# Performance work log

Measured on AMD Instinct MI355X. Metric: run time of the kernel, lower is better.

The kernel has to match this reference:

```python
import jax, jax.numpy as jnp
import numpy as np
from jax import lax


def _zc_rmsnorm(x, w, eps=1e-6):
    # ZeroCentredRMSNorm: scale is (1 + weight), weight init zeros
    v = jnp.mean(jnp.square(x), -1, keepdims=True)
    return x * lax.rsqrt(v + eps) * (1.0 + w)


def _short_conv(x, w, seg_id):
    # Depthwise causal conv (kernel=4, torch Conv1d tap layout) + silu,
    # respecting packed-segment boundaries (contributions from other
    # segments are masked out, matching varlen causal_conv1d).
    T = x.shape[0]
    out = x * w[:, 3]
    for s in range(1, 4):
        shifted = jnp.pad(x, ((s, 0), (0, 0)))[:T]
        same = jnp.pad(seg_id, (s, 0), constant_values=-1)[:T] == seg_id
        out = out + jnp.where(same[:, None], shifted, 0.0) * w[:, 3 - s]
    return jax.nn.silu(out)


def _l2norm(x, eps=1e-6):
    return x * lax.rsqrt(jnp.sum(jnp.square(x), -1, keepdims=True) + eps)


def _forward(x, ac_table, W_in, b_in, norm_w, Wq, Wk, Wv, conv_qw, conv_kw,
             conv_vw, Wb, Wa, A_log, dt_bias, Wg, o_norm_w, Wo, W_head, b_head,
             cu_seqlens, aircraft_type_idx):
    T = x.shape[0]
    NH = A_log.shape[0]
    # segment id per packed token
    seg_id = jnp.searchsorted(cu_seqlens, jnp.arange(T), side='right') - 1
    ac = ac_table[aircraft_type_idx]                    # [S, AC_D]
    h = jnp.concatenate([x, ac[seg_id]], axis=1) @ W_in + b_in  # [T, H]
    residual = h
    hn = _zc_rmsnorm(h, norm_w)
    # GatedDeltaNet projections + short conv + silu
    q = _short_conv(hn @ Wq, conv_qw, seg_id)           # [T, KD]
    k = _short_conv(hn @ Wk, conv_kw, seg_id)           # [T, KD]
    v = _short_conv(hn @ Wv, conv_vw, seg_id)           # [T, VD]
    HK = q.shape[1] // NH
    HV = v.shape[1] // NH
    q = _l2norm(q.reshape(T, NH, HK))
    k = _l2norm(k.reshape(T, NH, HK))
    v = v.reshape(T, NH, HV)
    beta = jax.nn.sigmoid(hn @ Wb)                      # [T, NH]
    g = -jnp.exp(A_log) * jax.nn.softplus(hn @ Wa + dt_bias)  # [T, NH] log-decay
    scale = HK ** -0.5
    # reset flag: 1.0 at the first token of each segment
    starts = jnp.zeros((T,), jnp.float32).at[cu_seqlens[:-1]].set(1.0)

    def step(S, inp):
        qt, kt, vt, gt, bt, rt = inp
        S = S * (1.0 - rt) * jnp.exp(gt)[:, None, None]       # decay (+ reset)
        kv = jnp.einsum('hk,hkv->hv', kt, S)                   # S^T k
        S = S + kt[:, :, None] * (bt[:, None] * (vt - kv))[:, None, :]
        return S, jnp.einsum('hk,hkv->hv', qt, S)

    S0 = jnp.zeros((NH, HK, HV), jnp.float32)
    _, o = lax.scan(step, S0, (q * scale, k, v, g, beta, starts))  # o: [T,NH,HV]
    # swish-gated RMSNorm on output heads
    gate = (hn @ Wg).reshape(T, NH, HV)
    o = o * lax.rsqrt(jnp.mean(jnp.square(o), -1, keepdims=True) + 1e-5) * o_norm_w
    o = o * gate * jax.nn.sigmoid(gate)
    h = o.reshape(T, NH * HV) @ Wo + residual
    pooled = h[cu_seqlens[1:] - 1]                      # 'last' pooling
    return pooled @ W_head + b_head                     # [S, 1]


def setup_inputs() -> dict:
    T, D_IN, H, NH, AC_N, AC_D, S = 32768, 16, 1024, 12, 64, 32, 16
    KD = int(H * 0.75)          # 768
    VD = KD * 2                 # 1536 (expand_v = 2)
    HK, HV = KD // NH, VD // NH # 64, 128
    rng = np.random.default_rng(0)
    interior = np.sort(rng.choice(np.arange(1, T), S - 1, replace=False))
    cu = jnp.asarray(np.concatenate([[0], interior, [T]]).astype(np.int32))
    ks = jax.random.split(jax.random.key(0), 24)

    def n(i, shape, s=0.02):
        return jax.random.normal(ks[i], shape, jnp.float32) * s

    return dict(
        x=jax.random.normal(ks[0], (T, D_IN), jnp.float32),
        cu_seqlens=cu,
        aircraft_type_idx=jax.random.randint(ks[1], (S,), 0, AC_N),
        ac_table=n(2, (AC_N, AC_D), 1.0),
        W_in=n(3, (D_IN + AC_D, H)), b_in=jnp.zeros((H,), jnp.float32),
        norm_w=jnp.zeros((H,), jnp.float32),
        Wq=n(4, (H, KD)), Wk=n(5, (H, KD)), Wv=n(6, (H, VD)),
        conv_qw=n(7, (KD, 4), 0.2), conv_kw=n(8, (KD, 4), 0.2),
        conv_vw=n(9, (VD, 4), 0.2),
        Wb=n(10, (H, NH)), Wa=n(11, (H, NH)),
        A_log=jnp.log(jax.random.uniform(ks[12], (NH,), jnp.float32, 1.0, 16.0)),
        dt_bias=n(13, (NH,), 0.1),
        Wg=n(14, (H, VD)), o_norm_w=jnp.ones((HV,), jnp.float32),
        Wo=n(15, (VD, H)),
        W_head=n(16, (H, 1)), b_head=jnp.zeros((1,), jnp.float32),
    )


def reference(x, cu_seqlens, aircraft_type_idx, ac_table, W_in, b_in, norm_w,
              Wq, Wk, Wv, conv_qw, conv_kw, conv_vw, Wb, Wa, A_log, dt_bias,
              Wg, o_norm_w, Wo, W_head, b_head):
    return _forward(x, ac_table, W_in, b_in, norm_w, Wq, Wk, Wv, conv_qw,
                    conv_kw, conv_vw, Wb, Wa, A_log, dt_bias, Wg, o_norm_w,
                    Wo, W_head, b_head, cu_seqlens, aircraft_type_idx)
```

## Files before the change

kernel.cpp:

```cpp
#include <hip/hip_runtime.h>
#include <stdint.h>

#define T_TOK 32768
#define H_DIM 1024
#define NH    12
#define HK    64
#define HV    128
#define KD    768
#define VD    1536
#define NSEG  16
#define NCOL  2432
#define FEAT  48
#define CHUNK_M 4096
#define NSLOT (T_TOK/8 + 32)
#define MAXSB 96
#define OCH   8

typedef unsigned int uint;
typedef unsigned short ushort;

typedef short bf16x8_t __attribute__((ext_vector_type(8)));
typedef float f32x4_t  __attribute__((ext_vector_type(4)));

__device__ __forceinline__ ushort f2b(float f){
  uint u = __float_as_uint(f);
  u += 0x7fffu + ((u>>16)&1u);
  return (ushort)(u>>16);
}
__device__ __forceinline__ float b2f(ushort u){ return __uint_as_float(((uint)u)<<16); }
__device__ __forceinline__ void unpack2(uint u, float&a, float&b){
  a = __uint_as_float(u<<16); b = __uint_as_float(u & 0xffff0000u);
}
__device__ __forceinline__ float sigm(float x){ return 1.f/(1.f + __expf(-x)); }
__device__ __forceinline__ float silu(float x){ return x * sigm(x); }

__global__ void segk(const int* __restrict__ cu, int* __restrict__ seg){
  int t = blockIdx.x*256 + threadIdx.x;
  if (t >= T_TOK) return;
  int s = 0;
  #pragma unroll
  for (int i=1;i<=NSEG;i++) s += (cu[i] <= t) ? 1 : 0;
  seg[t] = s;
}

__global__ __launch_bounds__(256,1) void stage_a(const float* __restrict__ x,
   const int* __restrict__ atype, const float* __restrict__ ac_table,
   const float* __restrict__ W_in, const float* __restrict__ b_in,
   const float* __restrict__ norm_w, const int* __restrict__ seg, int row_base,
   ushort* __restrict__ hn, float* __restrict__ h_end, float* __restrict__ hn_ends)
{
  __shared__ float feat[8][FEAT];
  __shared__ float hbuf[8][H_DIM];
  __shared__ float red[8];
  int tid = threadIdx.x;
  int base = row_base + blockIdx.x*8;
  int lbase = blockIdx.x*8;
  if (tid < 8) red[tid] = 0.f;
  for (int idx=tid; idx<8*FEAT; idx+=256){
    int rr = idx / FEAT, i = idx % FEAT;
    int t = base + rr;
    float v;
    if (i < 16) v = x[t*16 + i];
    else { int s = seg[t]; int a = atype[s]; v = ac_table[a*32 + (i-16)]; }
    feat[rr][i] = v;
  }
  __syncthreads();
  int c0 = tid*4;
  int lane = tid & 63;
  float4 bi = *(const float4*)&b_in[c0];
  for (int rc=0; rc<2; rc++){
    float acc[4][4];
    #pragma unroll
    for (int r4=0;r4<4;r4++){ acc[r4][0]=bi.x; acc[r4][1]=bi.y; acc[r4][2]=bi.z; acc[r4][3]=bi.w; }
    for (int i=0;i<FEAT;i++){
      float4 wu = *(const float4*)&W_in[i*H_DIM + c0];
      #pragma unroll
      for (int r4=0;r4<4;r4++){
        float f = feat[rc*4+r4][i];
        acc[r4][0] = fmaf(f,wu.x,acc[r4][0]);
        acc[r4][1] = fmaf(f,wu.y,acc[r4][1]);
        acc[r4][2] = fmaf(f,wu.z,acc[r4][2]);
        acc[r4][3] = fmaf(f,wu.w,acc[r4][3]);
      }
    }
    #pragma unroll
    for (int r4=0;r4<4;r4++){
      int rr = rc*4+r4;
      float sq = acc[r4][0]*acc[r4][0] + acc[r4][1]*acc[r4][1]
               + acc[r4][2]*acc[r4][2] + acc[r4][3]*acc[r4][3];
      #pragma unroll
      for (int off=1; off<64; off<<=1) sq += __shfl_xor(sq, off);
      if (lane==0) atomicAdd(&red[rr], sq);
      hbuf[rr][c0]=acc[r4][0]; hbuf[rr][c0+1]=acc[r4][1];
      hbuf[rr][c0+2]=acc[r4][2]; hbuf[rr][c0+3]=acc[r4][3];
    }
  }
  __syncthreads();
  float4 nw = *(const float4*)&norm_w[c0];
  for (int rr=0; rr<8; rr++){
    int t = base + rr;
    float sc = rsqrtf(red[rr]*(1.f/1024.f) + 1e-6f);
    float h0=hbuf[rr][c0], h1=hbuf[rr][c0+1], h2=hbuf[rr][c0+2], h3=hbuf[rr][c0+3];
    float n0=h0*sc*(1.f+nw.x), n1=h1*sc*(1.f+nw.y);
    float n2=h2*sc*(1.f+nw.z), n3=h3*sc*(1.f+nw.w);
    uint2 ov; ov.x = (uint)f2b(n0) | ((uint)f2b(n1)<<16);
    ov.y = (uint)f2b(n2) | ((uint)f2b(n3)<<16);
    *(uint2*)&hn[(size_t)(lbase+rr)*H_DIM + c0] = ov;
    int sgt = seg[t];
    bool isend = (t == T_TOK-1) || (seg[t+1] != sgt);
    if (isend){
      float* he = h_end + (size_t)sgt*H_DIM + c0;
      he[0]=h0; he[1]=h1; he[2]=h2; he[3]=h3;
    }
    #pragma unroll
    for (int d=0; d<4; d++){
      int td = t + d;
      if (td < T_TOK && seg[td] == sgt){
        bool end2 = (td == T_TOK-1) || (seg[td+1] != sgt);
        if (end2){
          float* hd = hn_ends + ((size_t)sgt*4 + (3-d))*H_DIM + c0;
          hd[0]=n0; hd[1]=n1; hd[2]=n2; hd[3]=n3;
        }
      }
    }
  }
}

__global__ void build_wt(const float* __restrict__ Wk, const float* __restrict__ Wv,
                         const float* __restrict__ Wb, const float* __restrict__ Wa,
                         ushort* __restrict__ wt)
{
  int idx = blockIdx.x*256 + threadIdx.x;
  int n = idx >> 10, k = idx & 1023;
  float v;
  if      (n < 768)  v = Wk[k*768 + n];
  else if (n < 2304) v = Wv[k*1536 + (n-768)];
  else if (n < 2316) v = Wb[k*12 + (n-2304)];
  else if (n < 2328) v = Wa[k*12 + (n-2316)];
  else               v = 0.f;
  wt[idx] = f2b(v);
}

__global__ __launch_bounds__(256,1) void gemm_bf16(const ushort* __restrict__ A,
    const ushort* __restrict__ Bt, int row_base,
    ushort* __restrict__ kpre, ushort* __restrict__ vpre, float* __restrict__ ba)
{
  const int K = H_DIM;
  __shared__ ushort As[128*40];
  __shared__ ushort Bs[128*40];
  int tid = threadIdx.x;
  const int ntile = NCOL >> 7;
  int mt = blockIdx.x / ntile, nt = blockIdx.x % ntile;
  int m0 = mt<<7, n0 = nt<<7;
  int r = tid>>2, c8 = (tid&3)<<3;
  const ushort* pa0 = A  + (size_t)(m0 + r)*K + c8;
  const ushort* pa1 = A  + (size_t)(m0 + r + 64)*K + c8;
  const ushort* pb0 = Bt + (size_t)(n0 + r)*K + c8;
  const ushort* pb1 = Bt + (size_t)(n0 + r + 64)*K + c8;
  int lane = tid & 63;
  int wv = tid >> 6; int wm = (wv>>1)<<6, wn = (wv&1)<<6;
  int mloc = lane & 15, q8 = (lane>>4)<<3;
  f32x4_t acc[4][4];
  f32x4_t zero = {0.f,0.f,0.f,0.f};
  #pragma unroll
  for (int i=0;i<4;i++)
    #pragma unroll
    for (int j=0;j<4;j++) acc[i][j] = zero;
  for (int kk=0; kk<K; kk+=32){
    uint4 a0 = *(const uint4*)(pa0 + kk);
    uint4 a1 = *(const uint4*)(pa1 + kk);
    uint4 b0 = *(const uint4*)(pb0 + kk);
    uint4 b1 = *(const uint4*)(pb1 + kk);
    __syncthreads();
    *(uint4*)&As[r*40 + c8] = a0;
    *(uint4*)&As[(r+64)*40 + c8] = a1;
    *(uint4*)&Bs[r*40 + c8] = b0;
    *(uint4*)&Bs[(r+64)*40 + c8] = b1;
    __syncthreads();
    bf16x8_t af[4], bfr[4];
    #pragma unroll
    for (int i=0;i<4;i++){
      af[i]  = *(const bf16x8_t*)&As[(wm + i*16 + mloc)*40 + q8];
      bfr[i] = *(const bf16x8_t*)&Bs[(wn + i*16 + mloc)*40 + q8];
    }
    #pragma unroll
    for (int i=0;i<4;i++)
      #pragma unroll
      for (int j=0;j<4;j++)
        acc[i][j] = __builtin_amdgcn_mfma_f32_16x16x32_bf16(af[i], bfr[j], acc[i][j], 0,0,0);
  }
  int rq = (lane>>4)<<2;
  if (nt < 18){
    ushort* dst; int nstr, cbase;
    if (nt < 6) { dst = kpre; nstr = KD; cbase = n0; }
    else        { dst = vpre; nstr = VD; cbase = n0 - KD; }
    #pragma unroll
    for (int i=0;i<4;i++){
      #pragma unroll
      for (int j=0;j<4;j++){
        int colg = cbase + wn + j*16 + mloc;
        #pragma unroll
        for (int rg=0; rg<4; rg++){
          int rowg = row_base + m0 + wm + i*16 + rq + rg;
          dst[(size_t)rowg*nstr + colg] = f2b(acc[i][j][rg]);
        }
      }
    }
  } else {
    #pragma unroll
    for (int i=0;i<4;i++){
      #pragma unroll
      for (int j=0;j<4;j++){
        int cl = wn + j*16 + mloc;
        if (cl >= 24) continue;
        #pragma unroll
        for (int rg=0; rg<4; rg++){
          int rowg = row_base + m0 + wm + i*16 + rq + rg;
          ba[(size_t)rowg*32 + cl] = acc[i][j][rg];
        }
      }
    }
  }
}

__global__ void dbk(const float* __restrict__ ba, const float* __restrict__ A_log,
                    const float* __restrict__ dt_bias, float2* __restrict__ db)
{
  int idx = blockIdx.x*256 + threadIdx.x;
  if (idx >= T_TOK*NH) return;
  int t = idx / NH, hh = idx % NH;
  float bp = ba[(size_t)t*32 + hh];
  float ap = ba[(size_t)t*32 + 12 + hh] + dt_bias[hh];
  float beta = sigm(bp);
  float sp = (ap > 20.f) ? ap : log1pf(__expf(ap));
  float dec = __expf(-__expf(A_log[hh]) * sp);
  float2 o; o.x = dec; o.y = beta;
  db[idx] = o;
}

__global__ void side_k(const ushort* __restrict__ kpre, const ushort* __restrict__ vpre,
                       ushort* __restrict__ side)
{
  int b = blockIdx.x;
  int base = b*64;
  for (int idx=threadIdx.x; idx<3*2304; idx+=256){
    int jrow = idx / 2304, c = idx % 2304;
    int t0 = base - 3 + jrow;
    ushort v = 0;
    if (t0 >= 0)
      v = (c < KD) ? kpre[(size_t)t0*KD + c] : vpre[(size_t)t0*VD + (c-KD)];
    side[(size_t)(b*3 + jrow)*2304 + c] = v;
  }
}

__global__ __launch_bounds__(256,1) void conv_ip(ushort* __restrict__ kpre,
   ushort* __restrict__ vpre, const ushort* __restrict__ side,
   const int* __restrict__ seg, const float* __restrict__ ckw, const float* __restrict__ cvw)
{
  int tid = threadIdx.x;
  int b = blockIdx.x;
  int base = b * 64;
  float w[9][4];
  int cj[9];
  #pragma unroll
  for (int j=0;j<9;j++){
    int c = tid + 256*j;
    cj[j] = c;
    float4 wu = (c < KD) ? *(const float4*)&ckw[c*4] : *(const float4*)&cvw[(c-KD)*4];
    w[j][0]=wu.x; w[j][1]=wu.y; w[j][2]=wu.z; w[j][3]=wu.w;
  }
  float p[9][4];
  #pragma unroll
  for (int j=0;j<9;j++){
    p[j][1] = b2f(side[(size_t)(b*3+0)*2304 + cj[j]]);
    p[j][2] = b2f(side[(size_t)(b*3+1)*2304 + cj[j]]);
    p[j][3] = b2f(side[(size_t)(b*3+2)*2304 + cj[j]]);
  }
  int s1 = (base-3>=0) ? seg[base-3] : -1;
  int s2 = (base-2>=0) ? seg[base-2] : -1;
  int s3 = (base-1>=0) ? seg[base-1] : -1;
  int s0;
  for (int rr=0; rr<64; rr++){
    int t = base + rr;
    s0 = s1; s1 = s2; s2 = s3; s3 = seg[t];
    #pragma unroll
    for (int j=0;j<9;j++){
      p[j][0]=p[j][1]; p[j][1]=p[j][2]; p[j][2]=p[j][3];
      int c = cj[j];
      p[j][3] = (c < KD) ? b2f(kpre[(size_t)t*KD + c]) : b2f(vpre[(size_t)t*VD + (c-KD)]);
    }
    bool m0 = (s0==s3), m1 = (s1==s3), m2 = (s2==s3);
    #pragma unroll
    for (int j=0;j<9;j++){
      float val = p[j][3]*w[j][3];
      val += m2 ? p[j][2]*w[j][2] : 0.f;
      val += m1 ? p[j][1]*w[j][1] : 0.f;
      val += m0 ? p[j][0]*w[j][0] : 0.f;
      val = silu(val);
      int c = cj[j];
      if (j < 3){
        float sq = val*val;
        #pragma unroll
        for (int off=1; off<64; off<<=1) sq += __shfl_xor(sq, off);
        float kn = val * rsqrtf(sq + 1e-6f);
        kpre[(size_t)t*KD + c] = f2b(kn);
      } else {
        vpre[(size_t)t*VD + (c-KD)] = f2b(val);
      }
    }
  }
}

__global__ __launch_bounds__(256,1) void qpre_k(const float* __restrict__ hn_ends,
   const float* __restrict__ Wq, const int* __restrict__ cu, float* __restrict__ qpre)
{
  __shared__ float hrow[H_DIM];
  int tid = threadIdx.x;
  int s = blockIdx.x >> 2, rr = blockIdx.x & 3;
  int t = cu[s+1] - 4 + rr;
  if (t >= 0)
    *(float4*)&hrow[tid*4] = *(const float4*)&hn_ends[(size_t)(s*4+rr)*H_DIM + tid*4];
  __syncthreads();
  for (int j=0;j<3;j++){
    int c = tid + 256*j;
    float acc = 0.f;
    if (t >= 0){
      for (int i0=0; i0<H_DIM; i0++)
        acc = fmaf(hrow[i0], Wq[(size_t)i0*KD + c], acc);
    }
    qpre[(size_t)(s*4+rr)*KD + c] = acc;
  }
}

__global__ __launch_bounds__(256,1) void qfin_k(const float* __restrict__ qpre,
   const float* __restrict__ cqw, const int* __restrict__ cu, const int* __restrict__ seg,
   float* __restrict__ qf)
{
  int tid = threadIdx.x;
  int s = blockIdx.x;
  int te = cu[s+1]-1;
  for (int j=0;j<3;j++){
    int c = tid + 256*j;
    float4 wu = *(const float4*)&cqw[c*4];
    float wv_[4] = {wu.x, wu.y, wu.z, wu.w};
    float val = 0.f;
    #pragma unroll
    for (int rr=0; rr<4; rr++){
      int t = te - 3 + rr;
      bool ok = (t >= 0) && (seg[t] == s);
      float pv = qpre[(size_t)(s*4+rr)*KD + c];
      val += ok ? pv * wv_[rr] : 0.f;
    }
    val = silu(val);
    float sq = val*val;
    #pragma unroll
    for (int off=1; off<64; off<<=1) sq += __shfl_xor(sq, off);
    qf[(size_t)s*KD + c] = val * rsqrtf(sq + 1e-6f) * 0.125f;
  }
}

__global__ __launch_bounds__(64,1) void gq_k(const ushort* __restrict__ kpost,
   const float2* __restrict__ db, const int* __restrict__ cu, float* __restrict__ gbuf)
{
  __shared__ float kls[8][64];
  __shared__ float dls[8];
  __shared__ float bls[8];
  int slot = blockIdx.x, h = blockIdx.y;
  int s=-1, n=0, te=0, L=0, st0=0;
  for (int ss=0; ss<NSEG; ss++){
    int st = cu[ss], en = cu[ss+1];
    int base = (st>>3) + ss;
    int nb = (en - st + 7) >> 3;
    if (slot >= base && slot < base + nb){ s=ss; n=slot-base; te=en-1; L=en-st; st0=st; }
  }
  if (s < 0) return;
  int lane = threadIdx.x;
  int vl = lane>>3, kq = lane&7;
  int j = 8*n + vl;
  bool ok = j < L;
  int t = ok ? (te - j) : st0;
  uint4 kv = *(const uint4*)(kpost + (size_t)t*KD + h*HK + kq*8);
  float f0,f1,f2,f3,f4,f5,f6,f7;
  unpack2(kv.x,f0,f1); unpack2(kv.y,f2,f3); unpack2(kv.z,f4,f5); unpack2(kv.w,f6,f7);
  if (!ok){ f0=0;f1=0;f2=0;f3=0;f4=0;f5=0;f6=0;f7=0; }
  float4 w0; w0.x=f0; w0.y=f1; w0.z=f2; w0.w=f3;
  float4 w1; w1.x=f4; w1.y=f5; w1.z=f6; w1.w=f7;
  *(float4*)&kls[vl][kq*8]   = w0;
  *(float4*)&kls[vl][kq*8+4] = w1;
  if (kq==0){
    float dd = 1.f, bb = 0.f;
    if (ok){ float2 g = db[(size_t)t*NH + h]; dd = g.x; bb = g.y; }
    dls[vl] = dd; bls[vl] = bb;
  }
  __syncthreads();
  float out = 0.f;
  if (lane < 28){
    int i = 1, base = 0;
    while (lane >= base + i){ base += i; i++; }
    int m = lane - base;
    const float4* pm = (const float4*)kls[m];
    const float4* pi = (const float4*)kls[i];
    float g = 0.f;
    #pragma unroll
    for (int d=0; d<16; d++){
      float4 xa = pm[d], xb = pi[d];
      g += xa.x*xb.x + xa.y*xb.y + xa.z*xb.z + xa.w*xb.w;
    }
    float W = 1.f;
    for (int l=m; l<i; l++) W *= dls[l];
    out = W * bls[m] * g;
  } else if (lane < 36){
    int i0 = lane - 28;
    float P = 1.f;
    for (int l=0; l<=i0; l++) P *= dls[l];
    out = P;
  } else if (lane < 44){
    int m = lane - 36;
    float W = 1.f;
    for (int l=m; l<8; l++) W *= dls[l];
    out = W * bls[m];
  } else if (lane < 52){
    out = bls[lane-44];
  }
  if (lane < 52) gbuf[((size_t)slot*NH + h)*52 + lane] = out;
}

__device__ __forceinline__ int sb_locate(const int* cu, int slot,
   int& m, int& start, int& te, int& L, int& gb)
{
  int acc = 0;
  int sfound = -1;
  for (int ss=0; ss<NSEG; ss++){
    int st = cu[ss], en = cu[ss+1];
    int Ls = en - st, nb8 = (Ls+7)>>3, nsb = (nb8+63)>>6;
    if (slot >= acc && slot < acc + nsb){
      sfound = ss; m = slot - acc; start = st; te = en-1; L = Ls; gb = (st>>3)+ss;
    }
    acc += nsb;
  }
  return sfound;
}

__global__ __launch_bounds__(64,1) void msb_k(const ushort* __restrict__ kpost,
   const float* __restrict__ gbuf, const int* __restrict__ cu, float* __restrict__ mbuf)
{
  __shared__ float kls[2][8][64];
  int slot = blockIdx.x, h = blockIdx.y;
  int m, start, te, L, gb;
  int s = sb_locate(cu, slot, m, start, te, L, gb);
  if (s < 0) return;
  int nb8 = (L+7)>>3;
  int n0 = m*64, n1 = min(nb8, n0+64);
  int lane = threadIdx.x;
  int vl = lane>>3, kq = lane&7;
  const ushort* kb2 = kpost + h*HK + kq*8;
  float R[64];
  #pragma unroll
  for (int i=0;i<64;i++) R[i] = (lane==i) ? 1.f : 0.f;
  {
    int jj = 8*n0+vl; int td = (jj<L) ? (te-jj) : start;
    uint4 kv = *(const uint4*)(kb2 + (size_t)td*KD);
    float f0,f1,f2,f3,f4,f5,f6,f7;
    unpack2(kv.x,f0,f1); unpack2(kv.y,f2,f3); unpack2(kv.z,f4,f5); unpack2(kv.w,f6,f7);
    float4 wa; wa.x=f0; wa.y=f1; wa.z=f2; wa.w=f3;
    float4 wb; wb.x=f4; wb.y=f5; wb.z=f6; wb.w=f7;
    *(float4*)&kls[0][vl][kq*8]   = wa;
    *(float4*)&kls[0][vl][kq*8+4] = wb;
  }
  __syncthreads();
  int buf = 0;
  for (int n=n0; n<n1; n++){
    uint4 kvn;
    {
      int nn = (n+1<n1) ? n+1 : n;
      int jj = 8*nn+vl; int td = (jj<L) ? (te-jj) : start;
      kvn = *(const uint4*)(kb2 + (size_t)td*KD);
    }
    const float4* g4 = (const float4*)(gbuf + ((size_t)(gb+n)*NH + h)*52);
    float4 q0=g4[0], q1=g4[1], q2=g4[2], q3=g4[3], q4=g4[4], q5=g4[5], q6=g4[6],
           q7=g4[7], q8=g4[8], q9=g4[9], q10=g4[10];
    float aa[8];
    #pragma unroll
    for (int j=0;j<8;j++){
      const float4* kp = (const float4*)kls[buf][j];
      float ac0=0.f, ac1=0.f;
      #pragma unroll
      for (int b=0;b<16;b++){
        float4 kv4 = kp[b];
        ac0 = fmaf(kv4.x, R[4*b+0], ac0); ac1 = fmaf(kv4.y, R[4*b+1], ac1);
        ac0 = fmaf(kv4.z, R[4*b+2], ac0); ac1 = fmaf(kv4.w, R[4*b+3], ac1);
      }
      aa[j] = ac0 + ac1;
    }
    float a0=aa[0],a1=aa[1],a2=aa[2],a3=aa[3],a4=aa[4],a5=aa[5],a6=aa[6],a7=aa[7];
    float c0 = a0;
    float c1 = q7.x*a1 - q0.x*c0;
    float c2 = q7.y*a2 - q0.y*c0 - q0.z*c1;
    float c3 = q7.z*a3 - q0.w*c0 - q1.x*c1 - q1.y*c2;
    float c4 = q7.w*a4 - q1.z*c0 - q1.w*c1 - q2.x*c2 - q2.y*c3;
    float c5 = q8.x*a5 - q2.z*c0 - q2.w*c1 - q3.x*c2 - q3.y*c3 - q3.z*c4;
    float c6 = q8.y*a6 - q3.w*c0 - q4.x*c1 - q4.y*c2 - q4.z*c3 - q4.w*c4 - q5.x*c5;
    float c7 = q8.z*a7 - q5.y*c0 - q5.z*c1 - q5.w*c2 - q6.x*c3 - q6.y*c4 - q6.z*c5 - q6.w*c6;
    float g0 = q9.x*c0, g1 = q9.y*c1, g2 = q9.z*c2, g3 = q9.w*c3;
    float g4_= q10.x*c4, g5 = q10.y*c5, g6 = q10.z*c6, g7 = q10.w*c7;
    float P8 = q8.w;
    const float4* k0p=(const float4*)kls[buf][0]; const float4* k1p=(const float4*)kls[buf][1];
    const float4* k2p=(const float4*)kls[buf][2]; const float4* k3p=(const float4*)kls[buf][3];
    const float4* k4p=(const float4*)kls[buf][4]; const float4* k5p=(const float4*)kls[buf][5];
    const float4* k6p=(const float4*)kls[buf][6]; const float4* k7p=(const float4*)kls[buf][7];
    #pragma unroll
    for (int b=0;b<16;b++){
      float4 x0=k0p[b],x1=k1p[b],x2=k2p[b],x3=k3p[b],x4=k4p[b],x5=k5p[b],x6=k6p[b],x7=k7p[b];
      float r0=R[4*b+0]*P8, r1=R[4*b+1]*P8, r2=R[4*b+2]*P8, r3=R[4*b+3]*P8;
      r0=fmaf(-g0,x0.x,r0); r1=fmaf(-g0,x0.y,r1); r2=fmaf(-g0,x0.z,r2); r3=fmaf(-g0,x0.w,r3);
      r0=fmaf(-g1,x1.x,r0); r1=fmaf(-g1,x1.y,r1); r2=fmaf(-g1,x1.z,r2); r3=fmaf(-g1,x1.w,r3);
      r0=fmaf(-g2,x2.x,r0); r1=fmaf(-g2,x2.y,r1); r2=fmaf(-g2,x2.z,r2); r3=fmaf(-g2,x2.w,r3);
      r0=fmaf(-g3,x3.x,r0); r1=fmaf(-g3,x3.y,r1); r2=fmaf(-g3,x3.z,r2); r3=fmaf(-g3,x3.w,r3);
      r0=fmaf(-g4_,x4.x,r0); r1=fmaf(-g4_,x4.y,r1); r2=fmaf(-g4_,x4.z,r2); r3=fmaf(-g4_,x4.w,r3);
      r0=fmaf(-g5,x5.x,r0); r1=fmaf(-g5,x5.y,r1); r2=fmaf(-g5,x5.z,r2); r3=fmaf(-g5,x5.w,r3);
      r0=fmaf(-g6,x6.x,r0); r1=fmaf(-g6,x6.y,r1); r2=fmaf(-g6,x6.z,r2); r3=fmaf(-g6,x6.w,r3);
      r0=fmaf(-g7,x7.x,r0); r1=fmaf(-g7,x7.y,r1); r2=fmaf(-g7,x7.z,r2); r3=fmaf(-g7,x7.w,r3);
      R[4*b+0]=r0; R[4*b+1]=r1; R[4*b+2]=r2; R[4*b+3]=r3;
    }
    {
      float f0,f1,f2,f3,f4,f5,f6,f7;
      unpack2(kvn.x,f0,f1); unpack2(kvn.y,f2,f3); unpack2(kvn.z,f4,f5); unpack2(kvn.w,f6,f7);
      float4 wa; wa.x=f0; wa.y=f1; wa.z=f2; wa.w=f3;
      float4 wb; wb.x=f4; wb.y=f5; wb.z=f6; wb.w=f7;
      *(float4*)&kls[buf^1][vl][kq*8]   = wa;
      *(float4*)&kls[buf^1][vl][kq*8+4] = wb;
    }
    __syncthreads();
    buf ^= 1;
  }
  float* mp = mbuf + ((size_t)slot*NH + h)*4096 + (size_t)lane*64;
  #pragma unroll
  for (int b=0;b<16;b++){
    float4 o; o.x=R[4*b+0]; o.y=R[4*b+1]; o.z=R[4*b+2]; o.w=R[4*b+3];
    *(float4*)&mp[4*b] = o;
  }
}

__global__ __launch_bounds__(64,1) void chain_k(const float* __restrict__ mbuf,
   const float* __restrict__ qf, const int* __restrict__ cu, float* __restrict__ rbuf)
{
  __shared__ float lsr[64];
  int bid = blockIdx.x;
  int s = bid / NH, h = bid % NH;
  int start = cu[s], end = cu[s+1];
  int L = end - start, nb8 = (L+7)>>3, nsb = (nb8+63)>>6;
  int sbase = 0;
  for (int ss=0; ss<s; ss++){
    int Ls = cu[ss+1]-cu[ss];
    sbase += ((((Ls+7)>>3)+63)>>6);
  }
  int lane = threadIdx.x;
  lsr[lane] = qf[(size_t)s*KD + h*HK + lane];
  __syncthreads();
  float r[64];
  #pragma unroll
  for (int i=0;i<64;i++) r[i] = lsr[i];
  for (int mm=0; mm<nsb; mm++){
    int slot = sbase + mm;
    rbuf[((size_t)slot*NH + h)*64 + lane] = lsr[lane];
    if (mm+1 >= nsb) break;
    const float* mb = mbuf + ((size_t)slot*NH + h)*4096 + lane;
    float y = 0.f;
    #pragma unroll
    for (int col=0; col<64; col++)
      y = fmaf(mb[(size_t)col*64], r[col], y);
    __syncthreads();
    lsr[lane] = y;
    __syncthreads();
    #pragma unroll
    for (int i=0;i<64;i++) r[i] = lsr[i];
  }
}

__global__ __launch_bounds__(64,1) void scan3_k(const ushort* __restrict__ kpost,
   const float* __restrict__ gbuf, const float* __restrict__ rbuf,
   const int* __restrict__ cu, float* __restrict__ cbuf)
{
  int slot = blockIdx.x, h = blockIdx.y;
  int m, start, te, L, gb;
  int s = sb_locate(cu, slot, m, start, te, L, gb);
  if (s < 0) return;
  int nb8 = (L+7)>>3;
  int n0 = m*64, n1 = min(nb8, n0+64);
  int lane = threadIdx.x;
  int vl = lane>>3, kq = lane&7;
  const float* rp = rbuf + ((size_t)slot*NH + h)*64 + kq*8;
  float4 rA = *(const float4*)rp;
  float4 rB = *(const float4*)(rp+4);
  float r0=rA.x, r1=rA.y, r2=rA.z, r3=rA.w, r4=rB.x, r5=rB.y, r6=rB.z, r7=rB.w;
  const ushort* kb = kpost + h*HK + kq*8;
  for (int n=n0; n<n1; n++){
    const float4* g4 = (const float4*)(gbuf + ((size_t)(gb+n)*NH + h)*52);
    float4 q0=g4[0], q1=g4[1], q2=g4[2], q3=g4[3], q4=g4[4], q5=g4[5], q6=g4[6],
           q7=g4[7], q8=g4[8], q9=g4[9], q10=g4[10], q11=g4[11], q12=g4[12];
    int jj = 8*n + vl;
    bool ok = jj < L;
    int td = ok ? (te - jj) : start;
    uint4 kd = *(const uint4*)(kb + (size_t)td*KD);
    if (!ok){ kd.x=0; kd.y=0; kd.z=0; kd.w=0; }
    int tb = te - 8*n;
    int t0c = max(tb-0, start), t1c = max(tb-1, start), t2c = max(tb-2, start), t3c = max(tb-3, start);
    int t4c = max(tb-4, start), t5c = max(tb-5, start), t6c = max(tb-6, start), t7c = max(tb-7, start);
    uint4 km0 = *(const uint4*)(kb + (size_t)t0c*KD);
    uint4 km1 = *(const uint4*)(kb + (size_t)t1c*KD);
    uint4 km2 = *(const uint4*)(kb + (size_t)t2c*KD);
    uint4 km3 = *(const uint4*)(kb + (size_t)t3c*KD);
    uint4 km4 = *(const uint4*)(kb + (size_t)t4c*KD);
    uint4 km5 = *(const uint4*)(kb + (size_t)t5c*KD);
    uint4 km6 = *(const uint4*)(kb + (size_t)t6c*KD);
    uint4 km7 = *(const uint4*)(kb + (size_t)t7c*KD);
    float kk0,kk1,kk2,kk3,kk4,kk5,kk6,kk7;
    unpack2(kd.x, kk0, kk1); unpack2(kd.y, kk2, kk3);
    unpack2(kd.z, kk4, kk5); unpack2(kd.w, kk6, kk7);
    float pa = r0*kk0, pb = r1*kk1;
    pa = fmaf(r2, kk2, pa); pb = fmaf(r3, kk3, pb);
    pa = fmaf(r4, kk4, pa); pb = fmaf(r5, kk5, pb);
    pa = fmaf(r6, kk6, pa); pb = fmaf(r7, kk7, pb);
    float part = pa + pb;
    part += __shfl_xor(part, 1); part += __shfl_xor(part, 2); part += __shfl_xor(part, 4);
    float a0 = __shfl(part, 0*8+kq), a1 = __shfl(part, 1*8+kq);
    float a2 = __shfl(part, 2*8+kq), a3 = __shfl(part, 3*8+kq);
    float a4 = __shfl(part, 4*8+kq), a5 = __shfl(part, 5*8+kq);
    float a6 = __shfl(part, 6*8+kq), a7 = __shfl(part, 7*8+kq);
    float c0 = a0;
    float c1 = q7.x*a1 - q0.x*c0;
    float c2 = q7.y*a2 - q0.y*c0 - q0.z*c1;
    float c3 = q7.z*a3 - q0.w*c0 - q1.x*c1 - q1.y*c2;
    float c4 = q7.w*a4 - q1.z*c0 - q1.w*c1 - q2.x*c2 - q2.y*c3;
    float c5 = q8.x*a5 - q2.z*c0 - q2.w*c1 - q3.x*c2 - q3.y*c3 - q3.z*c4;
    float c6 = q8.y*a6 - q3.w*c0 - q4.x*c1 - q4.y*c2 - q4.z*c3 - q4.w*c4 - q5.x*c5;
    float c7 = q8.z*a7 - q5.y*c0 - q5.z*c1 - q5.w*c2 - q6.x*c3 - q6.y*c4 - q6.z*c5 - q6.w*c6;
    {
      float cw = vl==0?c0: vl==1?c1: vl==2?c2: vl==3?c3: vl==4?c4: vl==5?c5: vl==6?c6: c7;
      float bw = vl==0?q11.x: vl==1?q11.y: vl==2?q11.z: vl==3?q11.w:
                 vl==4?q12.x: vl==5?q12.y: vl==6?q12.z: q12.w;
      if (kq == 0 && jj < L) cbuf[(size_t)(te-jj)*NH + h] = bw*cw;
    }
    float g0 = q9.x*c0, g1 = q9.y*c1, g2 = q9.z*c2, g3 = q9.w*c3;
    float g4_= q10.x*c4, g5 = q10.y*c5, g6 = q10.z*c6, g7 = q10.w*c7;
    float P8 = q8.w;
    r0*=P8; r1*=P8; r2*=P8; r3*=P8; r4*=P8; r5*=P8; r6*=P8; r7*=P8;
    float e0,e1,e2,e3,e4,e5,e6,e7;
#define UPD(KM,GM) \
    unpack2(KM.x,e0,e1); unpack2(KM.y,e2,e3); unpack2(KM.z,e4,e5); unpack2(KM.w,e6,e7); \
    r0 = fmaf(-GM, e0, r0); r1 = fmaf(-GM, e1, r1); r2 = fmaf(-GM, e2, r2); r3 = fmaf(-GM, e3, r3); \
    r4 = fmaf(-GM, e4, r4); r5 = fmaf(-GM, e5, r5); r6 = fmaf(-GM, e6, r6); r7 = fmaf(-GM, e7, r7);
    UPD(km0,g0) UPD(km1,g1) UPD(km2,g2) UPD(km3,g3)
    UPD(km4,g4_) UPD(km5,g5) UPD(km6,g6) UPD(km7,g7)
#undef UPD
  }
}

__global__ void zerok(float* __restrict__ p, int n){
  int i = blockIdx.x*256 + threadIdx.x;
  if (i < n) p[i] = 0.f;
}

__global__ __launch_bounds__(128,1) void ogemv2_k(const ushort* __restrict__ vpost,
   const float* __restrict__ cbuf, const int* __restrict__ cu, float* __restrict__ obuf)
{
  int bid = blockIdx.x;
  int ch = bid % OCH;
  int sh = bid / OCH;
  int s = sh / NH, h = sh % NH;
  int start = cu[s], end = cu[s+1];
  int L = end - start;
  int clen = (L + OCH - 1) / OCH;
  int t0 = start + ch*clen;
  int t1 = min(end, t0 + clen);
  if (t0 >= t1) return;
  int v = threadIdx.x;
  const ushort* vp = vpost + h*HV + v;
  const float* cp = cbuf + h;
  float o0=0,o1=0,o2=0,o3=0,o4=0,o5=0,o6=0,o7=0;
  int t = t0;
  for (; t+8 <= t1; t+=8){
    o0 = fmaf(cp[(size_t)(t+0)*NH], b2f(vp[(size_t)(t+0)*VD]), o0);
    o1 = fmaf(cp[(size_t)(t+1)*NH], b2f(vp[(size_t)(t+1)*VD]), o1);
    o2 = fmaf(cp[(size_t)(t+2)*NH], b2f(vp[(size_t)(t+2)*VD]), o2);
    o3 = fmaf(cp[(size_t)(t+3)*NH], b2f(vp[(size_t)(t+3)*VD]), o3);
    o4 = fmaf(cp[(size_t)(t+4)*NH], b2f(vp[(size_t)(t+4)*VD]), o4);
    o5 = fmaf(cp[(size_t)(t+5)*NH], b2f(vp[(size_t)(t+5)*VD]), o5);
    o6 = fmaf(cp[(size_t)(t+6)*NH], b2f(vp[(size_t)(t+6)*VD]), o6);
    o7 = fmaf(cp[(size_t)(t+7)*NH], b2f(vp[(size_t)(t+7)*VD]), o7);
  }
  for (; t<t1; t++) o0 = fmaf(cp[(size_t)t*NH], b2f(vp[(size_t)t*VD]), o0);
  float o = ((o0+o1)+(o2+o3)) + ((o4+o5)+(o6+o7));
  atomicAdd(&obuf[(size_t)s*VD + h*HV + v], o);
}

__global__ __launch_bounds__(256,1) void gate_k(const float* __restrict__ obuf,
   const float* __restrict__ hn_ends, const float* __restrict__ Wg,
   const float* __restrict__ onw, const int* __restrict__ cu, float* __restrict__ og)
{
  __shared__ float red[4];
  __shared__ float hrow[H_DIM];
  int tid = threadIdx.x;
  int s = blockIdx.x / 6, ch = blockIdx.x % 6;
  int cc = ch*256 + tid;
  *(float4*)&hrow[tid*4] = *(const float4*)&hn_ends[(size_t)(s*4+3)*H_DIM + tid*4];
  float o = obuf[(size_t)s*VD + cc];
  float sq = o*o;
  #pragma unroll
  for (int off=1; off<64; off<<=1) sq += __shfl_xor(sq, off);
  int wv = tid>>6, lane = tid&63;
  if (lane==0) red[wv] = sq;
  __syncthreads();
  float ssum = (tid<128) ? (red[0]+red[1]) : (red[2]+red[3]);
  float onr = o * rsqrtf(ssum*(1.f/128.f) + 1e-5f) * onw[cc & 127];
  float acc = 0.f;
  for (int i0=0;i0<H_DIM;i0++)
    acc = fmaf(hrow[i0], Wg[(size_t)i0*VD + cc], acc);
  og[(size_t)s*VD + cc] = onr * acc * sigm(acc);
}

__global__ __launch_bounds__(256,1) void final_k(const float* __restrict__ og,
   const float* __restrict__ Wo, const float* __restrict__ h_end,
   const float* __restrict__ W_head, const float* __restrict__ b_head,
   float* __restrict__ out)
{
  __shared__ float ogs[VD];
  __shared__ float redp[4];
  int tid = threadIdx.x;
  int s = blockIdx.x;
  for (int j=tid; j<VD; j+=256) ogs[j] = og[(size_t)s*VD + j];
  __syncthreads();
  int c0 = tid*4;
  float4 hh4 = *(const float4*)&h_end[(size_t)s*H_DIM + c0];
  float acc0 = hh4.x, acc1 = hh4.y, acc2 = hh4.z, acc3 = hh4.w;
  for (int j=0;j<VD;j++){
    float ov = ogs[j];
    float4 wo = *(const float4*)&Wo[(size_t)j*H_DIM + c0];
    acc0 = fmaf(ov,wo.x,acc0); acc1 = fmaf(ov,wo.y,acc1);
    acc2 = fmaf(ov,wo.z,acc2); acc3 = fmaf(ov,wo.w,acc3);
  }
  float4 wh = *(const float4*)&W_head[c0];
  float p = acc0*wh.x + acc1*wh.y + acc2*wh.z + acc3*wh.w;
  #pragma unroll
  for (int off=1; off<64; off<<=1) p += __shfl_xor(p, off);
  int wv = tid>>6, lane = tid&63;
  if (lane==0) redp[wv] = p;
  __syncthreads();
  if (tid==0) out[s] = redp[0]+redp[1]+redp[2]+redp[3] + b_head[0];
}

extern "C" void kernel_launch(void* const* d_in, const int* in_sizes, int n_in,
                              void* d_out, int out_size, void* d_ws, size_t ws_size,
                              hipStream_t stream)
{
  const float* x      = (const float*)d_in[0];
  const int*   cu     = (const int*)  d_in[1];
  const int*   atype  = (const int*)  d_in[2];
  const float* ac_tab = (const float*)d_in[3];
  const float* W_in   = (const float*)d_in[4];
  const float* b_in   = (const float*)d_in[5];
  const float* norm_w = (const float*)d_in[6];
  const float* Wq     = (const float*)d_in[7];
  const float* Wk     = (const float*)d_in[8];
  const float* Wv     = (const float*)d_in[9];
  const float* cqw    = (const float*)d_in[10];
  const float* ckw    = (const float*)d_in[11];
  const float* cvw    = (const float*)d_in[12];
  const float* Wb     = (const float*)d_in[13];
  const float* Wa     = (const float*)d_in[14];
  const float* A_log  = (const float*)d_in[15];
  const float* dt_b   = (const float*)d_in[16];
  const float* Wg     = (const float*)d_in[17];
  const float* onw    = (const float*)d_in[18];
  const float* Wo     = (const float*)d_in[19];
  const float* W_head = (const float*)d_in[20];
  const float* b_head = (const float*)d_in[21];
  float* out = (float*)d_out;

  char* w = (char*)d_ws;
  int*    seg     = (int*)w;     w += (size_t)T_TOK*4;
  float*  h_end   = (float*)w;   w += (size_t)NSEG*H_DIM*4;
  float*  hn_ends = (float*)w;   w += (size_t)NSEG*4*H_DIM*4;
  float*  qpre    = (float*)w;   w += (size_t)NSEG*4*KD*4;
  float*  qf      = (float*)w;   w += (size_t)NSEG*KD*4;
  float*  obuf    = (float*)w;   w += (size_t)NSEG*VD*4;
  float*  og      = (float*)w;   w += (size_t)NSEG*VD*4;
  float2* db      = (float2*)w;  w += (size_t)T_TOK*NH*8;
  float*  ba      = (float*)w;   w += (size_t)T_TOK*32*4;
  ushort* wt      = (ushort*)w;  w += (size_t)NCOL*H_DIM*2;
  ushort* side    = (ushort*)w;  w += (size_t)(T_TOK/64)*3*2304*2;
  float*  cbuf    = (float*)w;   w += (size_t)T_TOK*NH*4;
  float*  gbuf    = (float*)w;   w += (size_t)NSLOT*NH*52*4;
  float*  mbuf    = (float*)w;   w += (size_t)MAXSB*NH*4096*4;
  float*  rbuf    = (float*)w;   w += (size_t)MAXSB*NH*64*4;
  ushort* hn_c    = (ushort*)w;  w += (size_t)CHUNK_M*H_DIM*2;
  ushort* kpre    = (ushort*)w;  w += (size_t)T_TOK*KD*2;
  ushort* vpre    = (ushort*)w;  w += (size_t)T_TOK*VD*2;

  hipLaunchKernelGGL(segk,     dim3(T_TOK/256),        dim3(256), 0, stream, cu, seg);
  hipLaunchKernelGGL(build_wt, dim3((NCOL*H_DIM)/256), dim3(256), 0, stream, Wk, Wv, Wb, Wa, wt);
  hipLaunchKernelGGL(zerok,    dim3((NSEG*VD+255)/256),dim3(256), 0, stream, obuf, NSEG*VD);
  for (int c = 0; c < T_TOK/CHUNK_M; c++){
    int row_base = c*CHUNK_M;
    hipLaunchKernelGGL(stage_a,  dim3(CHUNK_M/8), dim3(256), 0, stream,
                       x, atype, ac_tab, W_in, b_in, norm_w, seg, row_base, hn_c, h_end, hn_ends);
    hipLaunchKernelGGL(gemm_bf16, dim3((CHUNK_M/128)*(NCOL/128)), dim3(256), 0, stream,
                       hn_c, wt, row_base, kpre, vpre, ba);
  }
  hipLaunchKernelGGL(dbk,      dim3((T_TOK*NH)/256),   dim3(256), 0, stream, ba, A_log, dt_b, db);
  hipLaunchKernelGGL(side_k,   dim3(T_TOK/64),         dim3(256), 0, stream, kpre, vpre, side);
  hipLaunchKernelGGL(conv_ip,  dim3(T_TOK/64),         dim3(256), 0, stream, kpre, vpre, side, seg, ckw, cvw);
  hipLaunchKernelGGL(qpre_k,   dim3(NSEG*4),           dim3(256), 0, stream, hn_ends, Wq, cu, qpre);
  hipLaunchKernelGGL(qfin_k,   dim3(NSEG),             dim3(256), 0, stream, qpre, cqw, cu, seg, qf);
  hipLaunchKernelGGL(gq_k,     dim3(NSLOT, NH),        dim3(64),  0, stream, kpre, db, cu, gbuf);
  hipLaunchKernelGGL(msb_k,    dim3(MAXSB, NH),        dim3(64),  0, stream, kpre, gbuf, cu, mbuf);
  hipLaunchKernelGGL(chain_k,  dim3(NSEG*NH),          dim3(64),  0, stream, mbuf, qf, cu, rbuf);
  hipLaunchKernelGGL(scan3_k,  dim3(MAXSB, NH),        dim3(64),  0, stream, kpre, gbuf, rbuf, cu, cbuf);
  hipLaunchKernelGGL(ogemv2_k, dim3(NSEG*NH*OCH),      dim3(128), 0, stream, vpre, cbuf, cu, obuf);
  hipLaunchKernelGGL(gate_k,   dim3(NSEG*6),           dim3(256), 0, stream, obuf, hn_ends, Wg, onw, cu, og);
  hipLaunchKernelGGL(final_k,  dim3(NSEG),             dim3(256), 0, stream, og, Wo, h_end, W_head, b_head, out);
}
```

Measured before the change: 1.912 ms.

## Spread msb_k state matrix across 512 threads with shuffle-reduced dot products

The msb_k kernel previously held a full 64-column state row per thread in a single 64-thread block, doing long serial FMA chains. It now uses 8 wavefronts where each thread owns 8 elements of one column, computes partial dot products and reduces them with xor shuffles across 8 lanes. This cuts per-thread register pressure and the serial latency chain on this sequential scan kernel, at the cost of extra shuffles and block-wide syncs per step. Loading of the k tile into shared memory is now done as scalar bf16 loads per thread.

```diff
diff --git a/kernel.cpp b/kernel.cpp
--- a/kernel.cpp
+++ b/kernel.cpp
@@ -441,7 +441,7 @@
   return sfound;
 }
 
-__global__ __launch_bounds__(64,1) void msb_k(const ushort* __restrict__ kpost,
+__global__ __launch_bounds__(512,1) void msb_k(const ushort* __restrict__ kpost,
    const float* __restrict__ gbuf, const int* __restrict__ cu, float* __restrict__ mbuf)
 {
   __shared__ float kls[2][8][64];
@@ -451,48 +451,50 @@
   if (s < 0) return;
   int nb8 = (L+7)>>3;
   int n0 = m*64, n1 = min(nb8, n0+64);
-  int lane = threadIdx.x;
-  int vl = lane>>3, kq = lane&7;
-  const ushort* kb2 = kpost + h*HK + kq*8;
-  float R[64];
-  #pragma unroll
-  for (int i=0;i<64;i++) R[i] = (lane==i) ? 1.f : 0.f;
+  int tid = threadIdx.x;
+  int lane = tid & 63;
+  int wv = tid >> 6;
+  int cl = lane >> 3, kq = lane & 7;
+  int col = wv*8 + cl;
+  int d0 = kq*8;
+  const ushort* kbase = kpost + h*HK;
+  float r0 = (d0+0==col)?1.f:0.f, r1 = (d0+1==col)?1.f:0.f;
+  float r2 = (d0+2==col)?1.f:0.f, r3 = (d0+3==col)?1.f:0.f;
+  float r4 = (d0+4==col)?1.f:0.f, r5 = (d0+5==col)?1.f:0.f;
+  float r6 = (d0+6==col)?1.f:0.f, r7 = (d0+7==col)?1.f:0.f;
   {
-    int jj = 8*n0+vl; int td = (jj<L) ? (te-jj) : start;
-    uint4 kv = *(const uint4*)(kb2 + (size_t)td*KD);
-    float f0,f1,f2,f3,f4,f5,f6,f7;
-    unpack2(kv.x,f0,f1); unpack2(kv.y,f2,f3); unpack2(kv.z,f4,f5); unpack2(kv.w,f6,f7);
-    float4 wa; wa.x=f0; wa.y=f1; wa.z=f2; wa.w=f3;
-    float4 wb; wb.x=f4; wb.y=f5; wb.z=f6; wb.w=f7;
-    *(float4*)&kls[0][vl][kq*8]   = wa;
-    *(float4*)&kls[0][vl][kq*8+4] = wb;
+    int jj = 8*n0 + wv; int td = (jj<L) ? (te-jj) : start;
+    kls[0][wv][lane] = b2f(kbase[(size_t)td*KD + lane]);
   }
   __syncthreads();
   int buf = 0;
   for (int n=n0; n<n1; n++){
-    uint4 kvn;
     {
       int nn = (n+1<n1) ? n+1 : n;
-      int jj = 8*nn+vl; int td = (jj<L) ? (te-jj) : start;
-      kvn = *(const uint4*)(kb2 + (size_t)td*KD);
+      int jj = 8*nn + wv; int td = (jj<L) ? (te-jj) : start;
+      kls[buf^1][wv][lane] = b2f(kbase[(size_t)td*KD + lane]);
     }
     const float4* g4 = (const float4*)(gbuf + ((size_t)(gb+n)*NH + h)*52);
     float4 q0=g4[0], q1=g4[1], q2=g4[2], q3=g4[3], q4=g4[4], q5=g4[5], q6=g4[6],
            q7=g4[7], q8=g4[8], q9=g4[9], q10=g4[10];
-    float aa[8];
-    #pragma unroll
-    for (int j=0;j<8;j++){
-      const float4* kp = (const float4*)kls[buf][j];
-      float ac0=0.f, ac1=0.f;
-      #pragma unroll
-      for (int b=0;b<16;b++){
-        float4 kv4 = kp[b];
-        ac0 = fmaf(kv4.x, R[4*b+0], ac0); ac1 = fmaf(kv4.y, R[4*b+1], ac1);
-        ac0 = fmaf(kv4.z, R[4*b+2], ac0); ac1 = fmaf(kv4.w, R[4*b+3], ac1);
-      }
-      aa[j] = ac0 + ac1;
-    }
-    float a0=aa[0],a1=aa[1],a2=aa[2],a3=aa[3],a4=aa[4],a5=aa[5],a6=aa[6],a7=aa[7];
+    float a0,a1,a2,a3,a4,a5,a6,a7;
+#define DOTJ(J, A) { \
+    float4 ka = *(const float4*)&kls[buf][J][d0]; \
+    float4 kbv = *(const float4*)&kls[buf][J][d0+4]; \
+    float xx = ka.x*r0 + ka.y*r1; \
+    xx = fmaf(ka.z, r2, xx); xx = fmaf(ka.w, r3, xx); \
+    xx = fmaf(kbv.x, r4, xx); xx = fmaf(kbv.y, r5, xx); \
+    xx = fmaf(kbv.z, r6, xx); xx = fmaf(kbv.w, r7, xx); \
+    A = xx; }
+    DOTJ(0,a0) DOTJ(1,a1) DOTJ(2,a2) DOTJ(3,a3)
+    DOTJ(4,a4) DOTJ(5,a5) DOTJ(6,a6) DOTJ(7,a7)
+#undef DOTJ
+    a0 += __shfl_xor(a0,1); a1 += __shfl_xor(a1,1); a2 += __shfl_xor(a2,1); a3 += __shfl_xor(a3,1);
+    a4 += __shfl_xor(a4,1); a5 += __shfl_xor(a5,1); a6 += __shfl_xor(a6,1); a7 += __shfl_xor(a7,1);
+    a0 += __shfl_xor(a0,2); a1 += __shfl_xor(a1,2); a2 += __shfl_xor(a2,2); a3 += __shfl_xor(a3,2);
+    a4 += __shfl_xor(a4,2); a5 += __shfl_xor(a5,2); a6 += __shfl_xor(a6,2); a7 += __shfl_xor(a7,2);
+    a0 += __shfl_xor(a0,4); a1 += __shfl_xor(a1,4); a2 += __shfl_xor(a2,4); a3 += __shfl_xor(a3,4);
+    a4 += __shfl_xor(a4,4); a5 += __shfl_xor(a5,4); a6 += __shfl_xor(a6,4); a7 += __shfl_xor(a7,4);
     float c0 = a0;
     float c1 = q7.x*a1 - q0.x*c0;
     float c2 = q7.y*a2 - q0.y*c0 - q0.z*c1;
@@ -504,41 +506,25 @@
     float g0 = q9.x*c0, g1 = q9.y*c1, g2 = q9.z*c2, g3 = q9.w*c3;
     float g4_= q10.x*c4, g5 = q10.y*c5, g6 = q10.z*c6, g7 = q10.w*c7;
     float P8 = q8.w;
-    const float4* k0p=(const float4*)kls[buf][0]; const float4* k1p=(const float4*)kls[buf][1];
-    const float4* k2p=(const float4*)kls[buf][2]; const float4* k3p=(const float4*)kls[buf][3];
-    const float4* k4p=(const float4*)kls[buf][4]; const float4* k5p=(const float4*)kls[buf][5];
-    const float4* k6p=(const float4*)kls[buf][6]; const float4* k7p=(const float4*)kls[buf][7];
-    #pragma unroll
-    for (int b=0;b<16;b++){
-      float4 x0=k0p[b],x1=k1p[b],x2=k2p[b],x3=k3p[b],x4=k4p[b],x5=k5p[b],x6=k6p[b],x7=k7p[b];
-      float r0=R[4*b+0]*P8, r1=R[4*b+1]*P8, r2=R[4*b+2]*P8, r3=R[4*b+3]*P8;
-      r0=fmaf(-g0,x0.x,r0); r1=fmaf(-g0,x0.y,r1); r2=fmaf(-g0,x0.z,r2); r3=fmaf(-g0,x0.w,r3);
-      r0=fmaf(-g1,x1.x,r0); r1=fmaf(-g1,x1.y,r1); r2=fmaf(-g1,x1.z,r2); r3=fmaf(-g1,x1.w,r3);
-      r0=fmaf(-g2,x2.x,r0); r1=fmaf(-g2,x2.y,r1); r2=fmaf(-g2,x2.z,r2); r3=fmaf(-g2,x2.w,r3);
-      r0=fmaf(-g3,x3.x,r0); r1=fmaf(-g3,x3.y,r1); r2=fmaf(-g3,x3.z,r2); r3=fmaf(-g3,x3.w,r3);
-      r0=fmaf(-g4_,x4.x,r0); r1=fmaf(-g4_,x4.y,r1); r2=fmaf(-g4_,x4.z,r2); r3=fmaf(-g4_,x4.w,r3);
-      r0=fmaf(-g5,x5.x,r0); r1=fmaf(-g5,x5.y,r1); r2=fmaf(-g5,x5.z,r2); r3=fmaf(-g5,x5.w,r3);
-      r0=fmaf(-g6,x6.x,r0); r1=fmaf(-g6,x6.y,r1); r2=fmaf(-g6,x6.z,r2); r3=fmaf(-g6,x6.w,r3);
-      r0=fmaf(-g7,x7.x,r0); r1=fmaf(-g7,x7.y,r1); r2=fmaf(-g7,x7.z,r2); r3=fmaf(-g7,x7.w,r3);
-      R[4*b+0]=r0; R[4*b+1]=r1; R[4*b+2]=r2; R[4*b+3]=r3;
-    }
-    {
-      float f0,f1,f2,f3,f4,f5,f6,f7;
-      unpack2(kvn.x,f0,f1); unpack2(kvn.y,f2,f3); unpack2(kvn.z,f4,f5); unpack2(kvn.w,f6,f7);
-      float4 wa; wa.x=f0; wa.y=f1; wa.z=f2; wa.w=f3;
-      float4 wb; wb.x=f4; wb.y=f5; wb.z=f6; wb.w=f7;
-      *(float4*)&kls[buf^1][vl][kq*8]   = wa;
-      *(float4*)&kls[buf^1][vl][kq*8+4] = wb;
-    }
+    r0*=P8; r1*=P8; r2*=P8; r3*=P8; r4*=P8; r5*=P8; r6*=P8; r7*=P8;
+#define UPDJ(J, G) { \
+    float4 ka = *(const float4*)&kls[buf][J][d0]; \
+    float4 kbv = *(const float4*)&kls[buf][J][d0+4]; \
+    r0 = fmaf(-(G), ka.x, r0); r1 = fmaf(-(G), ka.y, r1); \
+    r2 = fmaf(-(G), ka.z, r2); r3 = fmaf(-(G), ka.w, r3); \
+    r4 = fmaf(-(G), kbv.x, r4); r5 = fmaf(-(G), kbv.y, r5); \
+    r6 = fmaf(-(G), kbv.z, r6); r7 = fmaf(-(G), kbv.w, r7); }
+    UPDJ(0,g0) UPDJ(1,g1) UPDJ(2,g2) UPDJ(3,g3)
+    UPDJ(4,g4_) UPDJ(5,g5) UPDJ(6,g6) UPDJ(7,g7)
+#undef UPDJ
     __syncthreads();
     buf ^= 1;
   }
-  float* mp = mbuf + ((size_t)slot*NH + h)*4096 + (size_t)lane*64;
-  #pragma unroll
-  for (int b=0;b<16;b++){
-    float4 o; o.x=R[4*b+0]; o.y=R[4*b+1]; o.z=R[4*b+2]; o.w=R[4*b+3];
-    *(float4*)&mp[4*b] = o;
-  }
+  float* mp = mbuf + ((size_t)slot*NH + h)*4096 + (size_t)col*64 + d0;
+  float4 oA; oA.x=r0; oA.y=r1; oA.z=r2; oA.w=r3;
+  float4 oB; oB.x=r4; oB.y=r5; oB.z=r6; oB.w=r7;
+  *(float4*)&mp[0] = oA;
+  *(float4*)&mp[4] = oB;
 }
 
 __global__ __launch_bounds__(64,1) void chain_k(const float* __restrict__ mbuf,
@@ -813,7 +799,7 @@
   hipLaunchKernelGGL(qpre_k,   dim3(NSEG*4),           dim3(256), 0, stream, hn_ends, Wq, cu, qpre);
   hipLaunchKernelGGL(qfin_k,   dim3(NSEG),             dim3(256), 0, stream, qpre, cqw, cu, seg, qf);
   hipLaunchKernelGGL(gq_k,     dim3(NSLOT, NH),        dim3(64),  0, stream, kpre, db, cu, gbuf);
-  hipLaunchKernelGGL(msb_k,    dim3(MAXSB, NH),        dim3(64),  0, stream, kpre, gbuf, cu, mbuf);
+  hipLaunchKernelGGL(msb_k,    dim3(MAXSB, NH),        dim3(512), 0, stream, kpre, gbuf, cu, mbuf);
   hipLaunchKernelGGL(chain_k,  dim3(NSEG*NH),          dim3(64),  0, stream, mbuf, qf, cu, rbuf);
   hipLaunchKernelGGL(scan3_k,  dim3(MAXSB, NH),        dim3(64),  0, stream, kpre, gbuf, rbuf, cu, cbuf);
   hipLaunchKernelGGL(ogemv2_k, dim3(NSEG*NH*OCH),      dim3(128), 0, stream, vpre, cbuf, cu, obuf);
```

Result: faster. 1.593 ms (-16.7%).
